# Kernel optimization log

Measured on AMD Instinct MI355X. Metric: run time of the kernel, lower is better.

Reference implementation:

```python
import jax, jax.numpy as jnp
import numpy as np

B, S, D, H, P = 2, 2048, 1024, 16, 2048  # batch, q_len, d_model, heads, past_len
DEPTH = D // H
W_STD = 0.02


def setup_inputs() -> dict:
    key = jax.random.key(0)
    ks = jax.random.split(key, 5)
    x = jax.random.normal(ks[0], (B, S, D), dtype=jnp.float32)
    past_layer = jax.random.normal(ks[1], (B, 2, H, P, DEPTH), dtype=jnp.float32)
    w_attn = jax.random.normal(ks[2], (D, 3 * D), dtype=jnp.float32) * W_STD
    b_attn = jnp.zeros((3 * D,), dtype=jnp.float32)
    w_proj = jax.random.normal(ks[3], (D, D), dtype=jnp.float32) * W_STD
    b_proj = jnp.zeros((D,), dtype=jnp.float32)
    # causal mask with KV cache: query i sits at absolute position P+i; key j
    # is masked (1.0 -> +(-1e9)) when j > P + i.
    q_pos = P + jnp.arange(S)[:, None]        # [S,1]
    k_pos = jnp.arange(P + S)[None, :]        # [1,P+S]
    mask = (k_pos > q_pos).astype(jnp.float32)[None, None]  # [1,1,S,P+S]
    return {"x": x, "mask": mask, "past_layer": past_layer,
            "w_attn": w_attn, "b_attn": b_attn,
            "w_proj": w_proj, "b_proj": b_proj}


def _split_heads(t):
    # [B,S,D] -> [B,H,S,depth]
    b, s, _ = t.shape
    return t.reshape(b, s, H, DEPTH).transpose(0, 2, 1, 3)


def reference(x, mask, past_layer, w_attn, b_attn, w_proj, b_proj):
    # fused QKV projection (Conv1d == pointwise Linear)
    qkv = jnp.einsum('bsd,de->bse', x, w_attn) + b_attn        # [B,S,3D]
    q, k, v = jnp.split(qkv, 3, axis=2)
    q, k, v = _split_heads(q), _split_heads(k), _split_heads(v)
    # KV-cache concat
    k = jnp.concatenate([past_layer[:, 0], k], axis=2)         # [B,H,P+S,depth]
    v = jnp.concatenate([past_layer[:, 1], v], axis=2)
    present = jnp.stack([k, v], axis=1)                        # [B,2,H,P+S,depth]
    # scaled dot-product attention (full score matrix, eval mode: no dropout)
    scores = jnp.einsum('bhqd,bhkd->bhqk', q, k) / jnp.sqrt(
        jnp.asarray(DEPTH, dtype=jnp.float32))
    scores = scores + mask * (-1e9)
    attn = jax.nn.softmax(scores, axis=-1)
    ctx = jnp.einsum('bhqk,bhkd->bhqd', attn, v)               # [B,H,S,depth]
    merged = ctx.transpose(0, 2, 1, 3).reshape(B, S, D)
    output = jnp.einsum('bsd,de->bse', merged, w_proj) + b_proj
    return output, present
```

## Files before the change

kernel.cpp:

```cpp
#include <hip/hip_runtime.h>
#include <hip/hip_bf16.h>

#define B_ 2
#define S_ 2048
#define D_ 1024
#define H_ 16
#define P_ 2048
#define T_ 4096
#define DEPTH_ 64

typedef __bf16 bf16x8 __attribute__((ext_vector_type(8)));
typedef float  f32x4  __attribute__((ext_vector_type(4)));
typedef short  short8_t __attribute__((ext_vector_type(8)));
typedef unsigned short ushort_t;
typedef unsigned short ushort4_t __attribute__((ext_vector_type(4)));

__device__ __forceinline__ ushort_t f2bf(float f) {
    union { float f; unsigned u; } v; v.f = f;
    return (ushort_t)((v.u + 0x7fffu + ((v.u >> 16) & 1u)) >> 16);
}

__device__ __forceinline__ unsigned cvt_pk_bf16(float lo, float hi) {
    unsigned r;
    asm("v_cvt_pk_bf16_f32 %0, %1, %2" : "=v"(r) : "v"(lo), "v"(hi));
    return r;
}

__device__ __forceinline__ void gload16(const void* g, void* l) {
    __builtin_amdgcn_global_load_lds(
        (const __attribute__((address_space(1))) unsigned int*)g,
        (__attribute__((address_space(3))) unsigned int*)l, 16, 0, 0);
}

__global__ __launch_bounds__(256)
void convert_bf16_kernel(const float4* __restrict__ in, ushort4_t* __restrict__ out, int n4)
{
    for (int i = blockIdx.x * 256 + threadIdx.x; i < n4; i += gridDim.x * 256) {
        float4 v = in[i];
        ushort4_t o;
        o[0] = f2bf(v.x); o[1] = f2bf(v.y); o[2] = f2bf(v.z); o[3] = f2bf(v.w);
        out[i] = o;
    }
}

__global__ __launch_bounds__(256)
void transpose_conv_kernel(const float* __restrict__ w, ushort_t* __restrict__ wt, int N)
{
    __shared__ float t[64][65];
    const int tid = threadIdx.x;
    const int k0 = blockIdx.y * 64, n0 = blockIdx.x * 64;
    #pragma unroll
    for (int rep = 0; rep < 4; ++rep) {
        const int idx = rep * 256 + tid;
        const int r = idx >> 4, c = idx & 15;
        float4 v = *(const float4*)&w[(size_t)(k0 + r) * N + n0 + c * 4];
        t[r][c*4+0] = v.x; t[r][c*4+1] = v.y; t[r][c*4+2] = v.z; t[r][c*4+3] = v.w;
    }
    __syncthreads();
    #pragma unroll
    for (int rep = 0; rep < 4; ++rep) {
        const int idx = rep * 256 + tid;
        const int nl = idx >> 4, kg = idx & 15;
        ushort4_t o;
        o[0] = f2bf(t[kg*4+0][nl]); o[1] = f2bf(t[kg*4+1][nl]);
        o[2] = f2bf(t[kg*4+2][nl]); o[3] = f2bf(t[kg*4+3][nl]);
        *(ushort4_t*)&wt[(size_t)(n0 + nl) * 1024 + k0 + kg*4] = o;
    }
}

template<int MODE>
__global__ __launch_bounds__(256)
void gemm_bf16_kernel(const ushort_t* __restrict__ A,
                      const ushort_t* __restrict__ Bt,
                      const float*  __restrict__ bias,
                      ushort_t* __restrict__ out_qb,
                      float*  __restrict__ out_present,
                      float*  __restrict__ out_plain)
{
    __shared__ __attribute__((aligned(16))) ushort_t As[128*32];
    __shared__ __attribute__((aligned(16))) ushort_t Bs[128*32];

    const int tid  = threadIdx.x;
    const int w    = tid >> 6;
    const int lane = tid & 63;
    const int g    = lane >> 4;
    const int ln   = lane & 15;
    const int wr   = w >> 1, wc = w & 1;
    const int row0 = blockIdx.y * 128;
    const int col0 = blockIdx.x * 128;

    int srow[2], sgl[2];
    #pragma unroll
    for (int r = 0; r < 2; ++r) {
        const int o = (w*2 + r) * 1024 + lane * 16;
        srow[r] = o >> 6;
        const int gp = (o >> 4) & 3;
        sgl[r] = gp ^ ((srow[r] >> 1) & 3);
    }

    f32x4 acc[4][4];
    #pragma unroll
    for (int i = 0; i < 4; ++i)
        #pragma unroll
        for (int j = 0; j < 4; ++j)
            acc[i][j] = (f32x4){0.f, 0.f, 0.f, 0.f};

    for (int k0 = 0; k0 < 1024; k0 += 32) {
        #pragma unroll
        for (int r = 0; r < 2; ++r) {
            const int lb = (w*2 + r) * 512;
            gload16(&A [(size_t)(row0 + srow[r]) * 1024 + k0 + sgl[r]*8], &As[lb]);
            gload16(&Bt[(size_t)(col0 + srow[r]) * 1024 + k0 + sgl[r]*8], &Bs[lb]);
        }
        __syncthreads();

        bf16x8 af[4], bfr[4];
        #pragma unroll
        for (int i = 0; i < 4; ++i) {
            const int ra = wr*64 + i*16 + ln;
            const int ga = g ^ ((ra >> 1) & 3);
            af[i] = __builtin_bit_cast(bf16x8, *(const short8_t*)&As[ra*32 + ga*8]);
            const int rb = wc*64 + i*16 + ln;
            const int gb = g ^ ((rb >> 1) & 3);
            bfr[i] = __builtin_bit_cast(bf16x8, *(const short8_t*)&Bs[rb*32 + gb*8]);
        }
        #pragma unroll
        for (int i = 0; i < 4; ++i)
            #pragma unroll
            for (int j = 0; j < 4; ++j)
                acc[i][j] = __builtin_amdgcn_mfma_f32_16x16x32_bf16(af[i], bfr[j], acc[i][j], 0, 0, 0);
        __syncthreads();
    }

    #pragma unroll
    for (int i = 0; i < 4; ++i) {
        #pragma unroll
        for (int j = 0; j < 4; ++j) {
            const int rm = row0 + wr*64 + i*16 + g*4 + j;
            const int b  = rm >> 11;
            const int s  = rm & 2047;
            #pragma unroll
            for (int jn = 0; jn < 4; ++jn) {
                const int e = col0 + wc*64 + jn*16 + ln;
                const float v = acc[i][jn][j] + bias[e];
                if (MODE == 0) {
                    const int which = e >> 10;
                    const int f = e & 1023;
                    const int h = f >> 6, d = f & 63;
                    if (which == 0) {
                        out_qb[(size_t)(((b*16 + h) * 2048 + s) << 6) + d] =
                            f2bf(v * 0.18033688f);
                    } else {
                        const int kv = which - 1;
                        out_present[((((size_t)(b*2 + kv)*16 + h) * 4096 + 2048 + s) << 6) + d] = v;
                    }
                } else {
                    out_plain[(size_t)rm * 1024 + e] = v;
                }
            }
        }
    }
}

__global__ __launch_bounds__(256)
void prep_kv_kernel(const float* __restrict__ past,
                    float* __restrict__ present,
                    ushort_t* __restrict__ Kws, ushort_t* __restrict__ Vws)
{
    __shared__ float tv[64][65];
    const int tid = threadIdx.x;
    const int kt  = blockIdx.x;
    const int bh  = blockIdx.y;
    const int b   = bh >> 4, h = bh & 15;
    const bool old = (kt < 32);

    const float* Kp = old ? past    + (((size_t)(b*2+0)*16 + h) * P_ + kt*64) * 64
                          : present + (((size_t)(b*2+0)*16 + h) * T_ + kt*64) * 64;
    const float* Vp = old ? past    + (((size_t)(b*2+1)*16 + h) * P_ + kt*64) * 64
                          : present + (((size_t)(b*2+1)*16 + h) * T_ + kt*64) * 64;
    float4* PKo = (float4*)(present + (((size_t)(b*2+0)*16 + h) * T_ + kt*64) * 64);
    float4* PVo = (float4*)(present + (((size_t)(b*2+1)*16 + h) * T_ + kt*64) * 64);
    ushort_t* Kd = Kws + ((size_t)bh * T_ + kt*64) * 64;

    #pragma unroll
    for (int rep = 0; rep < 4; ++rep) {
        const int idx = rep * 256 + tid;
        float4 v = ((const float4*)Kp)[idx];
        if (old) PKo[idx] = v;
        ushort4_t o;
        o[0] = f2bf(v.x); o[1] = f2bf(v.y); o[2] = f2bf(v.z); o[3] = f2bf(v.w);
        *(ushort4_t*)&Kd[idx*4] = o;
        float4 vv = ((const float4*)Vp)[idx];
        if (old) PVo[idx] = vv;
        const int r = idx >> 4, c = idx & 15;
        tv[r][c*4+0] = vv.x; tv[r][c*4+1] = vv.y;
        tv[r][c*4+2] = vv.z; tv[r][c*4+3] = vv.w;
    }
    __syncthreads();
    #pragma unroll
    for (int rep = 0; rep < 4; ++rep) {
        const int idx = rep * 256 + tid;
        const int d = idx >> 4, pg = idx & 15;
        ushort4_t o;
        o[0] = f2bf(tv[pg*4+0][d]); o[1] = f2bf(tv[pg*4+1][d]);
        o[2] = f2bf(tv[pg*4+2][d]); o[3] = f2bf(tv[pg*4+3][d]);
        *(ushort4_t*)&Vws[((size_t)bh*64 + d) * T_ + kt*64 + pg*4] = o;
    }
}

__global__ __launch_bounds__(256, 2)
void attn_v10_kernel(const ushort_t* __restrict__ qin,
                     const ushort_t* __restrict__ Kws,
                     const ushort_t* __restrict__ Vws,
                     ushort_t* __restrict__ merged)
{
    __shared__ __attribute__((aligned(16))) ushort_t Kb0[4096];
    __shared__ __attribute__((aligned(16))) ushort_t Kb1[4096];
    __shared__ __attribute__((aligned(16))) ushort_t Vb0[4096];
    __shared__ __attribute__((aligned(16))) ushort_t Vb1[4096];
    __shared__ __attribute__((aligned(16))) ushort_t Pb[128*64];

    const int tid  = threadIdx.x;
    const int w    = tid >> 6;
    const int lane = tid & 63;
    const int g    = lane >> 4;
    const int ln   = lane & 15;
    const int lnm  = ln & 7;
    const int lsub = lane >> 3;
    const int swz8 = ((lane & 7) ^ lsub) * 8;

    const int bid = (int)blockIdx.x;
    const int a   = bid & 7;
    const int m_c = (bid >> 3) & 31;
    const int j   = bid >> 8;
    const int bh  = a * 4 + (m_c & 3);
    const int c   = m_c >> 2;
    const int qblk = (j == 0) ? c : (15 - c);
    const int q0   = qblk * 128;
    const int b    = bh >> 4, h = bh & 15;

    const ushort_t* Kbase = Kws + (size_t)bh * T_ * 64;
    const ushort_t* Vbase = Vws + (size_t)bh * 64 * T_;
    const int nt = 34 + 2 * qblk;

    const int kgOff0 = ((w*16 + 0 + lsub) << 6) + swz8;
    const int kgOff1 = ((w*16 + 8 + lsub) << 6) + swz8;
    const size_t vgOff0 = (size_t)(w*16 + 0 + lsub) * T_ + swz8;
    const size_t vgOff1 = (size_t)(w*16 + 8 + lsub) * T_ + swz8;
    const int ldsOff0 = (w*2 + 0) * 512;
    const int ldsOff1 = (w*2 + 1) * 512;
    const int pRow0 = (w*32 + ln) * 64;
    const int pRow1 = (w*32 + 16 + ln) * 64;

    gload16(Kbase + kgOff0, &Kb0[ldsOff0]);
    gload16(Kbase + kgOff1, &Kb0[ldsOff1]);
    gload16(Vbase + vgOff0, &Vb0[ldsOff0]);
    gload16(Vbase + vgOff1, &Vb0[ldsOff1]);

    bf16x8 qf[2][2];
    #pragma unroll
    for (int qg = 0; qg < 2; ++qg) {
        const ushort_t* Qr = qin + ((size_t)bh * S_ + q0 + w*32 + qg*16 + ln) * 64;
        #pragma unroll
        for (int kh = 0; kh < 2; ++kh)
            qf[qg][kh] = __builtin_bit_cast(bf16x8, *(const short8_t*)(Qr + kh*32 + g*8));
    }

    f32x4 o[2][4];
    #pragma unroll
    for (int qg = 0; qg < 2; ++qg)
        #pragma unroll
        for (int d = 0; d < 4; ++d) o[qg][d] = (f32x4){0.f, 0.f, 0.f, 0.f};
    float m = -3.0e38f;
    float l0 = 0.f, l1 = 0.f;

#define ATTN_BODY(KBUF, VBUF, NBUF_K, NBUF_V)                                   \
    {                                                                           \
        asm volatile("s_waitcnt vmcnt(2)" ::: "memory");                        \
        __builtin_amdgcn_s_barrier();                                           \
        __builtin_amdgcn_sched_barrier(0);                                      \
        const bool haspf = (t + 1 < nt);                                        \
        if (haspf) {                                                            \
            const size_t t0n = (size_t)(t + 1) * 64;                            \
            gload16(Kbase + (t0n << 6) + kgOff0, &NBUF_K[ldsOff0]);             \
            gload16(Kbase + (t0n << 6) + kgOff1, &NBUF_K[ldsOff1]);             \
            gload16(Vbase + vgOff0 + t0n, &NBUF_V[ldsOff0]);                    \
            gload16(Vbase + vgOff1 + t0n, &NBUF_V[ldsOff1]);                    \
            __builtin_amdgcn_sched_barrier(0);                                  \
        }                                                                       \
        f32x4 st[2][4];                                                         \
        __builtin_amdgcn_s_setprio(1);                                          \
        _Pragma("unroll")                                                       \
        for (int js = 0; js < 4; ++js) {                                        \
            const ushort_t* kr = &KBUF[(js*16 + ln) * 64];                      \
            bf16x8 a0 = __builtin_bit_cast(bf16x8, *(const short8_t*)(kr + ((    g) ^ lnm)*8)); \
            bf16x8 a1 = __builtin_bit_cast(bf16x8, *(const short8_t*)(kr + ((4 + g) ^ lnm)*8)); \
            _Pragma("unroll")                                                   \
            for (int qg = 0; qg < 2; ++qg) {                                    \
                f32x4 z = (f32x4){0.f, 0.f, 0.f, 0.f};                          \
                z = __builtin_amdgcn_mfma_f32_16x16x32_bf16(a0, qf[qg][0], z, 0, 0, 0); \
                z = __builtin_amdgcn_mfma_f32_16x16x32_bf16(a1, qf[qg][1], z, 0, 0, 0); \
                st[qg][js] = z;                                                 \
            }                                                                   \
        }                                                                       \
        __builtin_amdgcn_s_setprio(0);                                          \
        if (t >= nt - 2) {                                                      \
            const int off = t*64 - 2048 - q0;                                   \
            _Pragma("unroll")                                                   \
            for (int qg = 0; qg < 2; ++qg) {                                    \
                const int wrow = w*32 + qg*16 + ln;                             \
                _Pragma("unroll")                                               \
                for (int js = 0; js < 4; ++js)                                  \
                    _Pragma("unroll")                                           \
                    for (int r = 0; r < 4; ++r)                                 \
                        if (js*16 + g*4 + r + off > wrow) st[qg][js][r] = -1e30f; \
            }                                                                   \
        }                                                                       \
        float mx16 = st[0][0][0];                                               \
        _Pragma("unroll")                                                       \
        for (int qg = 0; qg < 2; ++qg)                                          \
            _Pragma("unroll")                                                   \
            for (int js = 0; js < 4; ++js) {                                    \
                float m01 = fmaxf(st[qg][js][0], st[qg][js][1]);                \
                float m23 = fmaxf(st[qg][js][2], st[qg][js][3]);                \
                mx16 = fmaxf(mx16, fmaxf(m01, m23));                            \
            }                                                                   \
        if (!__all(mx16 <= m + 8.0f)) {                                         \
            float gmx = fmaxf(mx16, __shfl_xor(mx16, 16));                      \
            gmx = fmaxf(gmx, __shfl_xor(gmx, 32));                              \
            const float mnew = fmaxf(m, gmx);                                   \
            const float corr = exp2f(m - mnew);                                 \
            m = mnew;                                                           \
            l0 *= corr; l1 *= corr;                                             \
            _Pragma("unroll")                                                   \
            for (int qg = 0; qg < 2; ++qg)                                      \
                _Pragma("unroll")                                               \
                for (int d = 0; d < 4; ++d)                                     \
                    _Pragma("unroll")                                           \
                    for (int r = 0; r < 4; ++r)                                 \
                        o[qg][d][r] *= corr;                                    \
        }                                                                       \
        _Pragma("unroll")                                                       \
        for (int qg = 0; qg < 2; ++qg) {                                        \
            const int pR = qg ? pRow1 : pRow0;                                  \
            float rs = 0.f;                                                     \
            _Pragma("unroll")                                                   \
            for (int js = 0; js < 4; ++js) {                                    \
                float p0 = exp2f(st[qg][js][0] - m);                            \
                float p1 = exp2f(st[qg][js][1] - m);                            \
                float p2 = exp2f(st[qg][js][2] - m);                            \
                float p3 = exp2f(st[qg][js][3] - m);                            \
                rs += (p0 + p1) + (p2 + p3);                                    \
                uint2 pk;                                                       \
                pk.x = cvt_pk_bf16(p0, p1);                                     \
                pk.y = cvt_pk_bf16(p2, p3);                                     \
                *(uint2*)&Pb[pR + (((js*4 + g) ^ (lnm << 1)) << 2)] = pk;       \
            }                                                                   \
            if (qg) l1 += rs; else l0 += rs;                                    \
        }                                                                       \
                                \
        if (haspf) { asm volatile("s_waitcnt vmcnt(4)" ::: "memory"); }         \
        else       { asm volatile("s_waitcnt vmcnt(0)" ::: "memory"); }         \
        __builtin_amdgcn_s_barrier();                                           \
        __builtin_amdgcn_sched_barrier(0);                                      \
        __builtin_amdgcn_s_setprio(1);                                          \
        _Pragma("unroll")                                                       \
        for (int kh = 0; kh < 2; ++kh) {                                        \
            bf16x8 pf0 = __builtin_bit_cast(bf16x8,                             \
                           *(const short8_t*)&Pb[pRow0 + (((kh*4 + g) ^ lnm) << 3)]); \
            bf16x8 pf1 = __builtin_bit_cast(bf16x8,                             \
                           *(const short8_t*)&Pb[pRow1 + (((kh*4 + g) ^ lnm) << 3)]); \
            _Pragma("unroll")                                                   \
            for (int dsub = 0; dsub < 4; ++dsub) {                              \
                const ushort_t* vr = &VBUF[(dsub*16 + ln) * 64];                \
                bf16x8 va = __builtin_bit_cast(bf16x8,                          \
                              *(const short8_t*)(vr + ((kh*4 + g) ^ lnm)*8));   \
                o[0][dsub] = __builtin_amdgcn_mfma_f32_16x16x32_bf16(va, pf0, o[0][dsub], 0, 0, 0); \
                o[1][dsub] = __builtin_amdgcn_mfma_f32_16x16x32_bf16(va, pf1, o[1][dsub], 0, 0, 0); \
            }                                                                   \
        }                                                                       \
        __builtin_amdgcn_s_setprio(0);                                          \
    }

    int t = 0;
    for (;;) {
        ATTN_BODY(Kb0, Vb0, Kb1, Vb1);
        if (++t == nt) break;
        ATTN_BODY(Kb1, Vb1, Kb0, Vb0);
        if (++t == nt) break;
    }
#undef ATTN_BODY

    float lf0 = l0 + __shfl_xor(l0, 16); lf0 += __shfl_xor(lf0, 32);
    float lf1 = l1 + __shfl_xor(l1, 16); lf1 += __shfl_xor(lf1, 32);
    #pragma unroll
    for (int qg = 0; qg < 2; ++qg) {
        const float inv = 1.f / (qg ? lf1 : lf0);
        const int row = q0 + w*32 + qg*16 + ln;
        #pragma unroll
        for (int dsub = 0; dsub < 4; ++dsub) {
            ushort4_t ov;
            ov[0] = f2bf(o[qg][dsub][0] * inv);
            ov[1] = f2bf(o[qg][dsub][1] * inv);
            ov[2] = f2bf(o[qg][dsub][2] * inv);
            ov[3] = f2bf(o[qg][dsub][3] * inv);
            *(ushort4_t*)&merged[((size_t)b * S_ + row) * D_ + h*64 + dsub*16 + g*4] = ov;
        }
    }
}

extern "C" void kernel_launch(void* const* d_in, const int* in_sizes, int n_in,
                              void* d_out, int out_size, void* d_ws, size_t ws_size,
                              hipStream_t stream)
{
    const float* x      = (const float*)d_in[0];
    const float* past   = (const float*)d_in[2];
    const float* w_attn = (const float*)d_in[3];
    const float* b_attn = (const float*)d_in[4];
    const float* w_proj = (const float*)d_in[5];
    const float* b_proj = (const float*)d_in[6];

    float* out     = (float*)d_out;
    float* present = out + (size_t)B_ * S_ * D_;

    ushort_t* wsu     = (ushort_t*)d_ws;
    ushort_t* q_ws    = wsu;
    ushort_t* mergedb = wsu + 4194304;
    ushort_t* wptb    = wsu + 8388608;
    ushort_t* xb      = wsu + 9437184;
    ushort_t* watb    = wsu + 13631488;
    ushort_t* K_ws    = wsu + 9437184;
    ushort_t* V_ws    = wsu + 17825792;

    convert_bf16_kernel<<<2048, 256, 0, stream>>>(
        (const float4*)x, (ushort4_t*)xb, (B_*S_*D_)/4);
    transpose_conv_kernel<<<dim3(48, 16), 256, 0, stream>>>(w_attn, watb, 3072);
    transpose_conv_kernel<<<dim3(16, 16), 256, 0, stream>>>(w_proj, wptb, 1024);

    gemm_bf16_kernel<0><<<dim3(24, 32), 256, 0, stream>>>(
        xb, watb, b_attn, q_ws, present, nullptr);

    prep_kv_kernel<<<dim3(64, 32), 256, 0, stream>>>(past, present, K_ws, V_ws);

    attn_v10_kernel<<<dim3(512), 256, 0, stream>>>(q_ws, K_ws, V_ws, mergedb);

    gemm_bf16_kernel<1><<<dim3(8, 32), 256, 0, stream>>>(
        mergedb, wptb, b_proj, nullptr, nullptr, out);
}
```

Baseline: 207.5 us.

## Software-pipeline attention: overlap previous tile's PV with current QK, 4-deep V ring

The attention loop is restructured so that the P·V MFMAs for tile t-1 are issued right after the QK^T MFMAs for tile t. This removes the second barrier and vmcnt wait that each iteration used to have between softmax and PV. V tiles are now prefetched two iterations ahead into a 4-entry LDS ring, while K keeps double buffering, and a final PV step runs after the loop. The aim is to hide softmax latency and global-load waits behind matrix work. The cost is more LDS per block (64KB instead of 48KB), which could pressure occupancy, plus more complex ring indexing.

Measured after the change: 204.1 us. Within noise of the previous version (-1.7%).

```diff
diff --git a/kernel.cpp b/kernel.cpp
--- a/kernel.cpp
+++ b/kernel.cpp
@@ -209,15 +209,13 @@
 }
 
 __global__ __launch_bounds__(256, 2)
-void attn_v10_kernel(const ushort_t* __restrict__ qin,
+void attn_v11_kernel(const ushort_t* __restrict__ qin,
                      const ushort_t* __restrict__ Kws,
                      const ushort_t* __restrict__ Vws,
                      ushort_t* __restrict__ merged)
 {
-    __shared__ __attribute__((aligned(16))) ushort_t Kb0[4096];
-    __shared__ __attribute__((aligned(16))) ushort_t Kb1[4096];
-    __shared__ __attribute__((aligned(16))) ushort_t Vb0[4096];
-    __shared__ __attribute__((aligned(16))) ushort_t Vb1[4096];
+    __shared__ __attribute__((aligned(16))) ushort_t Kb[2][4096];
+    __shared__ __attribute__((aligned(16))) ushort_t Vb[4][4096];
     __shared__ __attribute__((aligned(16))) ushort_t Pb[128*64];
 
     const int tid  = threadIdx.x;
@@ -252,10 +250,12 @@
     const int pRow0 = (w*32 + ln) * 64;
     const int pRow1 = (w*32 + 16 + ln) * 64;
 
-    gload16(Kbase + kgOff0, &Kb0[ldsOff0]);
-    gload16(Kbase + kgOff1, &Kb0[ldsOff1]);
-    gload16(Vbase + vgOff0, &Vb0[ldsOff0]);
-    gload16(Vbase + vgOff1, &Vb0[ldsOff1]);
+    gload16(Kbase + kgOff0, &Kb[0][ldsOff0]);
+    gload16(Kbase + kgOff1, &Kb[0][ldsOff1]);
+    gload16(Vbase + vgOff0, &Vb[0][ldsOff0]);
+    gload16(Vbase + vgOff1, &Vb[0][ldsOff1]);
+    gload16(Vbase + vgOff0 + 64, &Vb[1][ldsOff0]);
+    gload16(Vbase + vgOff1 + 64, &Vb[1][ldsOff1]);
 
     bf16x8 qf[2][2];
     #pragma unroll
@@ -274,25 +274,48 @@
     float m = -3.0e38f;
     float l0 = 0.f, l1 = 0.f;
 
-#define ATTN_BODY(KBUF, VBUF, NBUF_K, NBUF_V)                                   \
+    auto pv_step = [&](const ushort_t* vbase) {
+        __builtin_amdgcn_s_setprio(1);
+        #pragma unroll
+        for (int kh = 0; kh < 2; ++kh) {
+            bf16x8 pf0 = __builtin_bit_cast(bf16x8,
+                           *(const short8_t*)&Pb[pRow0 + (((kh*4 + g) ^ lnm) << 3)]);
+            bf16x8 pf1 = __builtin_bit_cast(bf16x8,
+                           *(const short8_t*)&Pb[pRow1 + (((kh*4 + g) ^ lnm) << 3)]);
+            #pragma unroll
+            for (int dsub = 0; dsub < 4; ++dsub) {
+                const ushort_t* vr = vbase + (dsub*16 + ln) * 64;
+                bf16x8 va = __builtin_bit_cast(bf16x8,
+                              *(const short8_t*)(vr + ((kh*4 + g) ^ lnm)*8));
+                o[0][dsub] = __builtin_amdgcn_mfma_f32_16x16x32_bf16(va, pf0, o[0][dsub], 0, 0, 0);
+                o[1][dsub] = __builtin_amdgcn_mfma_f32_16x16x32_bf16(va, pf1, o[1][dsub], 0, 0, 0);
+            }
+        }
+        __builtin_amdgcn_s_setprio(0);
+    };
+
+#define ATTN_STEP(KCUR, KNXT, VPRV, VISS)                                       \
     {                                                                           \
-        asm volatile("s_waitcnt vmcnt(2)" ::: "memory");                        \
+        if (t + 1 < nt) { asm volatile("s_waitcnt vmcnt(2)" ::: "memory"); }    \
+        else            { asm volatile("s_waitcnt vmcnt(0)" ::: "memory"); }    \
         __builtin_amdgcn_s_barrier();                                           \
         __builtin_amdgcn_sched_barrier(0);                                      \
-        const bool haspf = (t + 1 < nt);                                        \
-        if (haspf) {                                                            \
+        if (t + 1 < nt) {                                                       \
             const size_t t0n = (size_t)(t + 1) * 64;                            \
-            gload16(Kbase + (t0n << 6) + kgOff0, &NBUF_K[ldsOff0]);             \
-            gload16(Kbase + (t0n << 6) + kgOff1, &NBUF_K[ldsOff1]);             \
-            gload16(Vbase + vgOff0 + t0n, &NBUF_V[ldsOff0]);                    \
-            gload16(Vbase + vgOff1 + t0n, &NBUF_V[ldsOff1]);                    \
-            __builtin_amdgcn_sched_barrier(0);                                  \
-        }                                                                       \
+            gload16(Kbase + (t0n << 6) + kgOff0, &Kb[KNXT][ldsOff0]);           \
+            gload16(Kbase + (t0n << 6) + kgOff1, &Kb[KNXT][ldsOff1]);           \
+        }                                                                       \
+        if (t + 2 < nt) {                                                       \
+            const size_t t0v = (size_t)(t + 2) * 64;                            \
+            gload16(Vbase + vgOff0 + t0v, &Vb[VISS][ldsOff0]);                  \
+            gload16(Vbase + vgOff1 + t0v, &Vb[VISS][ldsOff1]);                  \
+        }                                                                       \
+        __builtin_amdgcn_sched_barrier(0);                                      \
         f32x4 st[2][4];                                                         \
         __builtin_amdgcn_s_setprio(1);                                          \
         _Pragma("unroll")                                                       \
         for (int js = 0; js < 4; ++js) {                                        \
-            const ushort_t* kr = &KBUF[(js*16 + ln) * 64];                      \
+            const ushort_t* kr = &Kb[KCUR][(js*16 + ln) * 64];                  \
             bf16x8 a0 = __builtin_bit_cast(bf16x8, *(const short8_t*)(kr + ((    g) ^ lnm)*8)); \
             bf16x8 a1 = __builtin_bit_cast(bf16x8, *(const short8_t*)(kr + ((4 + g) ^ lnm)*8)); \
             _Pragma("unroll")                                                   \
@@ -304,6 +327,8 @@
             }                                                                   \
         }                                                                       \
         __builtin_amdgcn_s_setprio(0);                                          \
+           \
+        if (t > 0) pv_step(&Vb[VPRV][0]);                                       \
         if (t >= nt - 2) {                                                      \
             const int off = t*64 - 2048 - q0;                                   \
             _Pragma("unroll")                                                   \
@@ -358,38 +383,22 @@
             }                                                                   \
             if (qg) l1 += rs; else l0 += rs;                                    \
         }                                                                       \
-                                \
-        if (haspf) { asm volatile("s_waitcnt vmcnt(4)" ::: "memory"); }         \
-        else       { asm volatile("s_waitcnt vmcnt(0)" ::: "memory"); }         \
-        __builtin_amdgcn_s_barrier();                                           \
-        __builtin_amdgcn_sched_barrier(0);                                      \
-        __builtin_amdgcn_s_setprio(1);                                          \
-        _Pragma("unroll")                                                       \
-        for (int kh = 0; kh < 2; ++kh) {                                        \
-            bf16x8 pf0 = __builtin_bit_cast(bf16x8,                             \
-                           *(const short8_t*)&Pb[pRow0 + (((kh*4 + g) ^ lnm) << 3)]); \
-            bf16x8 pf1 = __builtin_bit_cast(bf16x8,                             \
-                           *(const short8_t*)&Pb[pRow1 + (((kh*4 + g) ^ lnm) << 3)]); \
-            _Pragma("unroll")                                                   \
-            for (int dsub = 0; dsub < 4; ++dsub) {                              \
-                const ushort_t* vr = &VBUF[(dsub*16 + ln) * 64];                \
-                bf16x8 va = __builtin_bit_cast(bf16x8,                          \
-                              *(const short8_t*)(vr + ((kh*4 + g) ^ lnm)*8));   \
-                o[0][dsub] = __builtin_amdgcn_mfma_f32_16x16x32_bf16(va, pf0, o[0][dsub], 0, 0, 0); \
-                o[1][dsub] = __builtin_amdgcn_mfma_f32_16x16x32_bf16(va, pf1, o[1][dsub], 0, 0, 0); \
-            }                                                                   \
-        }                                                                       \
-        __builtin_amdgcn_s_setprio(0);                                          \
     }
 
     int t = 0;
     for (;;) {
-        ATTN_BODY(Kb0, Vb0, Kb1, Vb1);
+        ATTN_STEP(0, 1, 3, 2);
         if (++t == nt) break;
-        ATTN_BODY(Kb1, Vb1, Kb0, Vb0);
+        ATTN_STEP(1, 0, 0, 3);
         if (++t == nt) break;
-    }
-#undef ATTN_BODY
+        ATTN_STEP(0, 1, 1, 0);
+        if (++t == nt) break;
+        ATTN_STEP(1, 0, 2, 1);
+        if (++t == nt) break;
+    }
+#undef ATTN_STEP
+
+    pv_step(&Vb[(nt - 1) & 3][0]);
 
     float lf0 = l0 + __shfl_xor(l0, 16); lf0 += __shfl_xor(lf0, 32);
     float lf1 = l1 + __shfl_xor(l1, 16); lf1 += __shfl_xor(lf1, 32);
@@ -442,7 +451,7 @@
 
     prep_kv_kernel<<<dim3(64, 32), 256, 0, stream>>>(past, present, K_ws, V_ws);
 
-    attn_v10_kernel<<<dim3(512), 256, 0, stream>>>(q_ws, K_ws, V_ws, mergedb);
+    attn_v11_kernel<<<dim3(512), 256, 0, stream>>>(q_ws, K_ws, V_ws, mergedb);
 
     gemm_bf16_kernel<1><<<dim3(8, 32), 256, 0, stream>>>(
         mergedb, wptb, b_proj, nullptr, nullptr, out);
```

## Process 128-key tiles per attention step with split K/V prefetch schedule

Applied to the files above, without the earlier changes.

The attention loop now handles two 64-key sub-tiles per iteration, computing both QK score blocks before one shared online-softmax max update. This halves the number of rescale checks and barrier rounds per key. K is double-buffered across steps, while V is single-buffered per step and its next tile is only loaded after PV finishes. The intent is to amortise synchronisation and softmax bookkeeping over more MFMA work. The cost is more live registers for two score blocks and a V load that is exposed at the start of each step.

Result: no change. 207.7 us (+0.1%).

```diff
diff --git a/kernel.cpp b/kernel.cpp
--- a/kernel.cpp
+++ b/kernel.cpp
@@ -209,15 +209,13 @@
 }
 
 __global__ __launch_bounds__(256, 2)
-void attn_v10_kernel(const ushort_t* __restrict__ qin,
+void attn_v13_kernel(const ushort_t* __restrict__ qin,
                      const ushort_t* __restrict__ Kws,
                      const ushort_t* __restrict__ Vws,
                      ushort_t* __restrict__ merged)
 {
-    __shared__ __attribute__((aligned(16))) ushort_t Kb0[4096];
-    __shared__ __attribute__((aligned(16))) ushort_t Kb1[4096];
-    __shared__ __attribute__((aligned(16))) ushort_t Vb0[4096];
-    __shared__ __attribute__((aligned(16))) ushort_t Vb1[4096];
+    __shared__ __attribute__((aligned(16))) ushort_t Kb[2][2][4096];
+    __shared__ __attribute__((aligned(16))) ushort_t Vb[2][4096];
     __shared__ __attribute__((aligned(16))) ushort_t Pb[128*64];
 
     const int tid  = threadIdx.x;
@@ -241,7 +239,7 @@
 
     const ushort_t* Kbase = Kws + (size_t)bh * T_ * 64;
     const ushort_t* Vbase = Vws + (size_t)bh * 64 * T_;
-    const int nt = 34 + 2 * qblk;
+    const int nti = 17 + qblk;
 
     const int kgOff0 = ((w*16 + 0 + lsub) << 6) + swz8;
     const int kgOff1 = ((w*16 + 8 + lsub) << 6) + swz8;
@@ -252,10 +250,14 @@
     const int pRow0 = (w*32 + ln) * 64;
     const int pRow1 = (w*32 + 16 + ln) * 64;
 
-    gload16(Kbase + kgOff0, &Kb0[ldsOff0]);
-    gload16(Kbase + kgOff1, &Kb0[ldsOff1]);
-    gload16(Vbase + vgOff0, &Vb0[ldsOff0]);
-    gload16(Vbase + vgOff1, &Vb0[ldsOff1]);
+    gload16(Kbase + kgOff0,               &Kb[0][0][ldsOff0]);
+    gload16(Kbase + kgOff1,               &Kb[0][0][ldsOff1]);
+    gload16(Kbase + (64 << 6) + kgOff0,   &Kb[0][1][ldsOff0]);
+    gload16(Kbase + (64 << 6) + kgOff1,   &Kb[0][1][ldsOff1]);
+    gload16(Vbase + vgOff0,               &Vb[0][ldsOff0]);
+    gload16(Vbase + vgOff1,               &Vb[0][ldsOff1]);
+    gload16(Vbase + vgOff0 + 64,          &Vb[1][ldsOff0]);
+    gload16(Vbase + vgOff1 + 64,          &Vb[1][ldsOff1]);
 
     bf16x8 qf[2][2];
     #pragma unroll
@@ -274,56 +276,101 @@
     float m = -3.0e38f;
     float l0 = 0.f, l1 = 0.f;
 
-#define ATTN_BODY(KBUF, VBUF, NBUF_K, NBUF_V)                                   \
+#define QK_SUB(ST, KSRC)                                                        \
+    _Pragma("unroll")                                                           \
+    for (int js = 0; js < 4; ++js) {                                            \
+        const ushort_t* kr = &KSRC[(js*16 + ln) * 64];                          \
+        bf16x8 a0 = __builtin_bit_cast(bf16x8, *(const short8_t*)(kr + ((    g) ^ lnm)*8)); \
+        bf16x8 a1 = __builtin_bit_cast(bf16x8, *(const short8_t*)(kr + ((4 + g) ^ lnm)*8)); \
+        _Pragma("unroll")                                                       \
+        for (int qg = 0; qg < 2; ++qg) {                                        \
+            f32x4 z = (f32x4){0.f, 0.f, 0.f, 0.f};                              \
+            z = __builtin_amdgcn_mfma_f32_16x16x32_bf16(a0, qf[qg][0], z, 0, 0, 0); \
+            z = __builtin_amdgcn_mfma_f32_16x16x32_bf16(a1, qf[qg][1], z, 0, 0, 0); \
+            ST[qg][js] = z;                                                     \
+        }                                                                       \
+    }
+
+#define EXP_SUB(ST)                                                             \
+    _Pragma("unroll")                                                           \
+    for (int qg = 0; qg < 2; ++qg) {                                            \
+        const int pR = qg ? pRow1 : pRow0;                                      \
+        float rs = 0.f;                                                         \
+        _Pragma("unroll")                                                       \
+        for (int js = 0; js < 4; ++js) {                                        \
+            float p0 = exp2f(ST[qg][js][0] - m);                                \
+            float p1 = exp2f(ST[qg][js][1] - m);                                \
+            float p2 = exp2f(ST[qg][js][2] - m);                                \
+            float p3 = exp2f(ST[qg][js][3] - m);                                \
+            rs += (p0 + p1) + (p2 + p3);                                        \
+            uint2 pk;                                                           \
+            pk.x = cvt_pk_bf16(p0, p1);                                         \
+            pk.y = cvt_pk_bf16(p2, p3);                                         \
+            *(uint2*)&Pb[pR + (((js*4 + g) ^ (lnm << 1)) << 2)] = pk;           \
+        }                                                                       \
+        if (qg) l1 += rs; else l0 += rs;                                        \
+    }
+
+#define PV_SUB(VSRC)                                                            \
+    __builtin_amdgcn_s_setprio(1);                                              \
+    _Pragma("unroll")                                                           \
+    for (int kh = 0; kh < 2; ++kh) {                                            \
+        bf16x8 pf0 = __builtin_bit_cast(bf16x8,                                 \
+                       *(const short8_t*)&Pb[pRow0 + (((kh*4 + g) ^ lnm) << 3)]); \
+        bf16x8 pf1 = __builtin_bit_cast(bf16x8,                                 \
+                       *(const short8_t*)&Pb[pRow1 + (((kh*4 + g) ^ lnm) << 3)]); \
+        _Pragma("unroll")                                                       \
+        for (int dsub = 0; dsub < 4; ++dsub) {                                  \
+            const ushort_t* vr = &VSRC[(dsub*16 + ln) * 64];                    \
+            bf16x8 va = __builtin_bit_cast(bf16x8,                              \
+                          *(const short8_t*)(vr + ((kh*4 + g) ^ lnm)*8));       \
+            o[0][dsub] = __builtin_amdgcn_mfma_f32_16x16x32_bf16(va, pf0, o[0][dsub], 0, 0, 0); \
+            o[1][dsub] = __builtin_amdgcn_mfma_f32_16x16x32_bf16(va, pf1, o[1][dsub], 0, 0, 0); \
+        }                                                                       \
+    }                                                                           \
+    __builtin_amdgcn_s_setprio(0);
+
+#define ATTN_STEP(PAR)                                                          \
     {                                                                           \
-        asm volatile("s_waitcnt vmcnt(2)" ::: "memory");                        \
+        const bool haspf = (t + 1 < nti);                                       \
+        asm volatile("s_waitcnt vmcnt(4)" ::: "memory");         \
         __builtin_amdgcn_s_barrier();                                           \
         __builtin_amdgcn_sched_barrier(0);                                      \
-        const bool haspf = (t + 1 < nt);                                        \
-        if (haspf) {                                                            \
-            const size_t t0n = (size_t)(t + 1) * 64;                            \
-            gload16(Kbase + (t0n << 6) + kgOff0, &NBUF_K[ldsOff0]);             \
-            gload16(Kbase + (t0n << 6) + kgOff1, &NBUF_K[ldsOff1]);             \
-            gload16(Vbase + vgOff0 + t0n, &NBUF_V[ldsOff0]);                    \
-            gload16(Vbase + vgOff1 + t0n, &NBUF_V[ldsOff1]);                    \
+        if (haspf) {                              \
+            const size_t kBase = ((size_t)(t + 1) * 128) << 6;                  \
+            gload16(Kbase + kBase + kgOff0,             &Kb[PAR^1][0][ldsOff0]);\
+            gload16(Kbase + kBase + kgOff1,             &Kb[PAR^1][0][ldsOff1]);\
+            gload16(Kbase + kBase + (64 << 6) + kgOff0, &Kb[PAR^1][1][ldsOff0]);\
+            gload16(Kbase + kBase + (64 << 6) + kgOff1, &Kb[PAR^1][1][ldsOff1]);\
             __builtin_amdgcn_sched_barrier(0);                                  \
         }                                                                       \
-        f32x4 st[2][4];                                                         \
+        f32x4 stA[2][4], stB[2][4];                                             \
         __builtin_amdgcn_s_setprio(1);                                          \
-        _Pragma("unroll")                                                       \
-        for (int js = 0; js < 4; ++js) {                                        \
-            const ushort_t* kr = &KBUF[(js*16 + ln) * 64];                      \
-            bf16x8 a0 = __builtin_bit_cast(bf16x8, *(const short8_t*)(kr + ((    g) ^ lnm)*8)); \
-            bf16x8 a1 = __builtin_bit_cast(bf16x8, *(const short8_t*)(kr + ((4 + g) ^ lnm)*8)); \
-            _Pragma("unroll")                                                   \
-            for (int qg = 0; qg < 2; ++qg) {                                    \
-                f32x4 z = (f32x4){0.f, 0.f, 0.f, 0.f};                          \
-                z = __builtin_amdgcn_mfma_f32_16x16x32_bf16(a0, qf[qg][0], z, 0, 0, 0); \
-                z = __builtin_amdgcn_mfma_f32_16x16x32_bf16(a1, qf[qg][1], z, 0, 0, 0); \
-                st[qg][js] = z;                                                 \
-            }                                                                   \
-        }                                                                       \
+        QK_SUB(stA, Kb[PAR][0]);                                                \
+        QK_SUB(stB, Kb[PAR][1]);                                                \
         __builtin_amdgcn_s_setprio(0);                                          \
-        if (t >= nt - 2) {                                                      \
-            const int off = t*64 - 2048 - q0;                                   \
+        if (t == nti - 1) {            \
             _Pragma("unroll")                                                   \
             for (int qg = 0; qg < 2; ++qg) {                                    \
                 const int wrow = w*32 + qg*16 + ln;                             \
                 _Pragma("unroll")                                               \
                 for (int js = 0; js < 4; ++js)                                  \
                     _Pragma("unroll")                                           \
-                    for (int r = 0; r < 4; ++r)                                 \
-                        if (js*16 + g*4 + r + off > wrow) st[qg][js][r] = -1e30f; \
+                    for (int r = 0; r < 4; ++r) {                               \
+                        if (js*16 + g*4 + r      > wrow) stA[qg][js][r] = -1e30f; \
+                        if (js*16 + g*4 + r + 64 > wrow) stB[qg][js][r] = -1e30f; \
+                    }                                                           \
             }                                                                   \
         }                                                                       \
-        float mx16 = st[0][0][0];                                               \
+        float mx16 = stA[0][0][0];                                              \
         _Pragma("unroll")                                                       \
         for (int qg = 0; qg < 2; ++qg)                                          \
             _Pragma("unroll")                                                   \
             for (int js = 0; js < 4; ++js) {                                    \
-                float m01 = fmaxf(st[qg][js][0], st[qg][js][1]);                \
-                float m23 = fmaxf(st[qg][js][2], st[qg][js][3]);                \
-                mx16 = fmaxf(mx16, fmaxf(m01, m23));                            \
+                mx16 = fmaxf(mx16, fmaxf(fmaxf(stA[qg][js][0], stA[qg][js][1]), \
+                                         fmaxf(stA[qg][js][2], stA[qg][js][3]))); \
+                mx16 = fmaxf(mx16, fmaxf(fmaxf(stB[qg][js][0], stB[qg][js][1]), \
+                                         fmaxf(stB[qg][js][2], stB[qg][js][3]))); \
             }                                                                   \
         if (!__all(mx16 <= m + 8.0f)) {                                         \
             float gmx = fmaxf(mx16, __shfl_xor(mx16, 16));                      \
@@ -340,56 +387,36 @@
                     for (int r = 0; r < 4; ++r)                                 \
                         o[qg][d][r] *= corr;                                    \
         }                                                                       \
-        _Pragma("unroll")                                                       \
-        for (int qg = 0; qg < 2; ++qg) {                                        \
-            const int pR = qg ? pRow1 : pRow0;                                  \
-            float rs = 0.f;                                                     \
-            _Pragma("unroll")                                                   \
-            for (int js = 0; js < 4; ++js) {                                    \
-                float p0 = exp2f(st[qg][js][0] - m);                            \
-                float p1 = exp2f(st[qg][js][1] - m);                            \
-                float p2 = exp2f(st[qg][js][2] - m);                            \
-                float p3 = exp2f(st[qg][js][3] - m);                            \
-                rs += (p0 + p1) + (p2 + p3);                                    \
-                uint2 pk;                                                       \
-                pk.x = cvt_pk_bf16(p0, p1);                                     \
-                pk.y = cvt_pk_bf16(p2, p3);                                     \
-                *(uint2*)&Pb[pR + (((js*4 + g) ^ (lnm << 1)) << 2)] = pk;       \
-            }                                                                   \
-            if (qg) l1 += rs; else l0 += rs;                                    \
-        }                                                                       \
-                                \
+        EXP_SUB(stA);                                                           \
+             \
         if (haspf) { asm volatile("s_waitcnt vmcnt(4)" ::: "memory"); }         \
         else       { asm volatile("s_waitcnt vmcnt(0)" ::: "memory"); }         \
         __builtin_amdgcn_s_barrier();                                           \
         __builtin_amdgcn_sched_barrier(0);                                      \
-        __builtin_amdgcn_s_setprio(1);                                          \
-        _Pragma("unroll")                                                       \
-        for (int kh = 0; kh < 2; ++kh) {                                        \
-            bf16x8 pf0 = __builtin_bit_cast(bf16x8,                             \
-                           *(const short8_t*)&Pb[pRow0 + (((kh*4 + g) ^ lnm) << 3)]); \
-            bf16x8 pf1 = __builtin_bit_cast(bf16x8,                             \
-                           *(const short8_t*)&Pb[pRow1 + (((kh*4 + g) ^ lnm) << 3)]); \
-            _Pragma("unroll")                                                   \
-            for (int dsub = 0; dsub < 4; ++dsub) {                              \
-                const ushort_t* vr = &VBUF[(dsub*16 + ln) * 64];                \
-                bf16x8 va = __builtin_bit_cast(bf16x8,                          \
-                              *(const short8_t*)(vr + ((kh*4 + g) ^ lnm)*8));   \
-                o[0][dsub] = __builtin_amdgcn_mfma_f32_16x16x32_bf16(va, pf0, o[0][dsub], 0, 0, 0); \
-                o[1][dsub] = __builtin_amdgcn_mfma_f32_16x16x32_bf16(va, pf1, o[1][dsub], 0, 0, 0); \
-            }                                                                   \
-        }                                                                       \
-        __builtin_amdgcn_s_setprio(0);                                          \
+        PV_SUB(Vb[0]);           \
+        EXP_SUB(stB);           \
+        PV_SUB(Vb[1]);                                                          \
+        if (haspf) {                \
+            __builtin_amdgcn_s_barrier();                                       \
+            const size_t vKey = (size_t)(t + 1) * 128;                          \
+            gload16(Vbase + vgOff0 + vKey,      &Vb[0][ldsOff0]);               \
+            gload16(Vbase + vgOff1 + vKey,      &Vb[0][ldsOff1]);               \
+            gload16(Vbase + vgOff0 + vKey + 64, &Vb[1][ldsOff0]);               \
+            gload16(Vbase + vgOff1 + vKey + 64, &Vb[1][ldsOff1]);               \
+        }                                                                       \
     }
 
     int t = 0;
     for (;;) {
-        ATTN_BODY(Kb0, Vb0, Kb1, Vb1);
-        if (++t == nt) break;
-        ATTN_BODY(Kb1, Vb1, Kb0, Vb0);
-        if (++t == nt) break;
-    }
-#undef ATTN_BODY
+        ATTN_STEP(0);
+        if (++t == nti) break;
+        ATTN_STEP(1);
+        if (++t == nti) break;
+    }
+#undef ATTN_STEP
+#undef QK_SUB
+#undef EXP_SUB
+#undef PV_SUB
 
     float lf0 = l0 + __shfl_xor(l0, 16); lf0 += __shfl_xor(lf0, 32);
     float lf1 = l1 + __shfl_xor(l1, 16); lf1 += __shfl_xor(lf1, 32);
@@ -442,7 +469,7 @@
 
     prep_kv_kernel<<<dim3(64, 32), 256, 0, stream>>>(past, present, K_ws, V_ws);
 
-    attn_v10_kernel<<<dim3(512), 256, 0, stream>>>(q_ws, K_ws, V_ws, mergedb);
+    attn_v13_kernel<<<dim3(512), 256, 0, stream>>>(q_ws, K_ws, V_ws, mergedb);
 
     gemm_bf16_kernel<1><<<dim3(8, 32), 256, 0, stream>>>(
         mergedb, wptb, b_proj, nullptr, nullptr, out);
```
